# Kernel tuning notes

Hardware: AMD Instinct MI355X
Metric: run time of the kernel (lower is better)

Reference implementation:

```python
import jax, jax.numpy as jnp
import numpy as np

D_MODEL = 512
NHEAD = 8
HEAD_DIM = D_MODEL // NHEAD
A, B = 1024, 16


def setup_inputs() -> dict:
    key = jax.random.key(0)
    ks = jax.random.split(key, 6)
    s = 1.0 / np.sqrt(D_MODEL)
    return {
        "src": jax.random.normal(ks[0], (A, B, D_MODEL), jnp.float32),
        "asset_relation_bias": jax.random.normal(ks[1], (A, A), jnp.float32) * 0.1,
        "Wq": jax.random.normal(ks[2], (D_MODEL, D_MODEL), jnp.float32) * s,
        "bq": jnp.zeros((D_MODEL,), jnp.float32),
        "Wk": jax.random.normal(ks[3], (D_MODEL, D_MODEL), jnp.float32) * s,
        "bk": jnp.zeros((D_MODEL,), jnp.float32),
        "Wv": jax.random.normal(ks[4], (D_MODEL, D_MODEL), jnp.float32) * s,
        "bv": jnp.zeros((D_MODEL,), jnp.float32),
        "Wo": jax.random.normal(ks[5], (D_MODEL, D_MODEL), jnp.float32) * s,
        "bo": jnp.zeros((D_MODEL,), jnp.float32),
    }


def reference(src, asset_relation_bias, Wq, bq, Wk, bk, Wv, bv, Wo, bo):
    # src: [A, B, H]; attention is over the asset dim A.
    scale = HEAD_DIM ** -0.5

    def proj_heads(x, W, b):
        y = x @ W.T + b                      # [A, B, H]  (torch Linear: x @ W.T + b)
        y = y.reshape(A, B, NHEAD, HEAD_DIM)
        return jnp.transpose(y, (1, 2, 0, 3))  # [B, nh, A, hd]

    q = proj_heads(src, Wq, bq)
    k = proj_heads(src, Wk, bk)
    v = proj_heads(src, Wv, bv)

    logits = jnp.einsum("bnad,bnkd->bnak", q, k) * scale  # [B, nh, A, A]
    logits = logits + asset_relation_bias[None, None]     # additive relation bias
    attn = jax.nn.softmax(logits, axis=-1)                # dropout = identity (eval)
    out = jnp.einsum("bnak,bnkd->bnad", attn, v)          # [B, nh, A, hd]
    out = jnp.transpose(out, (2, 0, 1, 3)).reshape(A, B, D_MODEL)
    out = out @ Wo.T + bo
    return out
```

## Files before the change

kernel.cpp:

```cpp
#include <hip/hip_runtime.h>
#include <hip/hip_bf16.h>

#define A_DIM 1024
#define B_DIM 16
#define DM    512
#define NH    8
#define HD    64

#define LDT 72

typedef short s16x8 __attribute__((ext_vector_type(8)));
typedef float f32x4 __attribute__((ext_vector_type(4)));

static __device__ __forceinline__ unsigned short f2b(float f) {
    __hip_bfloat16 h = __float2bfloat16(f);
    unsigned short u;
    __builtin_memcpy(&u, &h, 2);
    return u;
}
static __device__ __forceinline__ uint2 cvt4(float4 v) {
    __hip_bfloat162 lo = __float22bfloat162_rn(make_float2(v.x, v.y));
    __hip_bfloat162 hi = __float22bfloat162_rn(make_float2(v.z, v.w));
    unsigned int ulo, uhi;
    __builtin_memcpy(&ulo, &lo, 4);
    __builtin_memcpy(&uhi, &hi, 4);
    return make_uint2(ulo, uhi);
}

__global__ __launch_bounds__(256) void qkv_gemm(
    const float* __restrict__ src,
    const float* __restrict__ Wq, const float* __restrict__ bq,
    const float* __restrict__ Wk, const float* __restrict__ bk,
    const float* __restrict__ Wv, const float* __restrict__ bv,
    short* __restrict__ Qb, short* __restrict__ Kb, short* __restrict__ Vb)
{
    __shared__ short As[128 * LDT];
    __shared__ short Bs[128 * LDT];

    const int tid  = threadIdx.x;
    const int wave = tid >> 6, lane = tid & 63;
    const int quad = lane >> 4, l16 = lane & 15;
    const int waveM = (wave >> 1) * 64, waveN = (wave & 1) * 64;
    const int mbase = blockIdx.y * 128;
    const int nbase = blockIdx.x * 128;
    const int mat   = nbase >> 9;
    const float* W    = (mat == 0) ? Wq : (mat == 1) ? Wk : Wv;
    const float* bvec = (mat == 0) ? bq : (mat == 1) ? bk : bv;
    short* dst        = (mat == 0) ? Qb : (mat == 1) ? Kb : Vb;
    const float oscale = (mat == 0) ? 0.125f : 1.0f;
    const int wrow0 = nbase & 511;

    f32x4 acc[4][4];
    #pragma unroll
    for (int i = 0; i < 4; i++)
        #pragma unroll
        for (int j = 0; j < 4; j++)
            acc[i][j] = (f32x4){0.f, 0.f, 0.f, 0.f};

    for (int kb = 0; kb < 8; ++kb) {
        __syncthreads();
        #pragma unroll
        for (int p = 0; p < 8; p++) {
            int chunk = tid + p * 256;
            int row = chunk >> 4, c = chunk & 15;
            float4 a4 = *(const float4*)&src[(mbase + row) * 512 + kb * 64 + c * 4];
            *(uint2*)&As[row * LDT + c * 4] = cvt4(a4);
            float4 w4 = *(const float4*)&W[(wrow0 + row) * 512 + kb * 64 + c * 4];
            *(uint2*)&Bs[row * LDT + c * 4] = cvt4(w4);
        }
        __syncthreads();
        #pragma unroll
        for (int k0i = 0; k0i < 2; k0i++) {
            s16x8 af[4], bf[4];
            #pragma unroll
            for (int mi = 0; mi < 4; mi++)
                af[mi] = *(const s16x8*)&As[(waveM + mi * 16 + l16) * LDT + (k0i * 4 + quad) * 8];
            #pragma unroll
            for (int ni = 0; ni < 4; ni++)
                bf[ni] = *(const s16x8*)&Bs[(waveN + ni * 16 + l16) * LDT + (k0i * 4 + quad) * 8];
            #pragma unroll
            for (int mi = 0; mi < 4; mi++)
                #pragma unroll
                for (int ni = 0; ni < 4; ni++)
                    acc[mi][ni] = __builtin_amdgcn_mfma_f32_16x16x32_bf16(
                        af[mi], bf[ni], acc[mi][ni], 0, 0, 0);
        }
    }

    #pragma unroll
    for (int mi = 0; mi < 4; mi++) {
        #pragma unroll
        for (int ni = 0; ni < 4; ni++) {
            #pragma unroll
            for (int r = 0; r < 4; r++) {
                int t = mbase + waveM + mi * 16 + quad * 4 + r;
                int o = wrow0 + waveN + ni * 16 + l16;
                float v = (acc[mi][ni][r] + bvec[o]) * oscale;
                int a = t >> 4, bb = t & 15, n = o >> 6, d = o & 63;
                dst[((bb * NH + n) * A_DIM + a) * HD + d] = (short)f2b(v);
            }
        }
    }
}

__global__ __launch_bounds__(256) void attn_kernel(
    const short* __restrict__ Qb, const short* __restrict__ Kb,
    const short* __restrict__ Vb, const float* __restrict__ bias,
    short* __restrict__ AO)
{
    __shared__ short Ks[64 * LDT];
    __shared__ short Vt[64 * LDT];
    __shared__ short Ps[4][16 * LDT];

    const int tid  = threadIdx.x;
    const int wave = tid >> 6, lane = tid & 63;
    const int quad = lane >> 4, l16 = lane & 15;
    const int bn = blockIdx.y;
    const int qrow0 = blockIdx.x * 64 + wave * 16;

    const short* Qg = Qb + bn * (A_DIM * HD);
    const short* Kg = Kb + bn * (A_DIM * HD);
    const short* Vg = Vb + bn * (A_DIM * HD);

    s16x8 qf[2];
    #pragma unroll
    for (int k0i = 0; k0i < 2; k0i++)
        qf[k0i] = *(const s16x8*)&Qg[(qrow0 + l16) * HD + k0i * 32 + quad * 8];

    float lsum[4];
    f32x4 of[4];
    #pragma unroll
    for (int r = 0; r < 4; r++) lsum[r] = 0.f;
    #pragma unroll
    for (int db = 0; db < 4; db++) of[db] = (f32x4){0.f, 0.f, 0.f, 0.f};

    for (int kb = 0; kb < 16; ++kb) {
        __syncthreads();
        #pragma unroll
        for (int p = 0; p < 2; p++) {
            int chunk = tid + p * 256;
            int row = chunk >> 3, c = chunk & 7;
            *(s16x8*)&Ks[row * LDT + c * 8] =
                *(const s16x8*)&Kg[(kb * 64 + row) * HD + c * 8];
            s16x8 vv = *(const s16x8*)&Vg[(kb * 64 + row) * HD + c * 8];
            #pragma unroll
            for (int j = 0; j < 8; j++) {
                int d = c * 8 + j;
                Vt[d * LDT + (((row >> 3) ^ c) << 3) + (row & 7)] = vv[j];
            }
        }
        __syncthreads();

        float sv[4][4];
        #pragma unroll
        for (int cb = 0; cb < 4; cb++) {
            f32x4 s = (f32x4){0.f, 0.f, 0.f, 0.f};
            #pragma unroll
            for (int k0i = 0; k0i < 2; k0i++) {
                s16x8 kf = *(const s16x8*)&Ks[(cb * 16 + l16) * LDT + (k0i * 4 + quad) * 8];
                s = __builtin_amdgcn_mfma_f32_16x16x32_bf16(qf[k0i], kf, s, 0, 0, 0);
            }
            #pragma unroll
            for (int r = 0; r < 4; r++) {
                int arow = qrow0 + quad * 4 + r;
                int kcol = kb * 64 + cb * 16 + l16;
                sv[cb][r] = s[r] + bias[arow * A_DIM + kcol];
            }
        }

        #pragma unroll
        for (int r = 0; r < 4; r++) {
            int prow = quad * 4 + r;
            #pragma unroll
            for (int cb = 0; cb < 4; cb++) {
                float pv = __expf(sv[cb][r]);
                lsum[r] += pv;
                Ps[wave][prow * LDT + cb * 16 + l16] = (short)f2b(pv);
            }
        }

        #pragma unroll
        for (int k0i = 0; k0i < 2; k0i++) {
            s16x8 pf = *(const s16x8*)&Ps[wave][l16 * LDT + (k0i * 4 + quad) * 8];
            #pragma unroll
            for (int db = 0; db < 4; db++) {
                int rr = db * 16 + l16;
                s16x8 vf = *(const s16x8*)&Vt[rr * LDT +
                            (((k0i * 4 + quad) ^ (rr >> 3)) << 3)];
                of[db] = __builtin_amdgcn_mfma_f32_16x16x32_bf16(pf, vf, of[db], 0, 0, 0);
            }
        }
    }

    #pragma unroll
    for (int r = 0; r < 4; r++) {
        float ps = lsum[r];
        ps += __shfl_xor(ps, 1);
        ps += __shfl_xor(ps, 2);
        ps += __shfl_xor(ps, 4);
        ps += __shfl_xor(ps, 8);
        lsum[r] = 1.0f / ps;
    }

    const int b = bn >> 3, n = bn & 7;
    #pragma unroll
    for (int db = 0; db < 4; db++) {
        #pragma unroll
        for (int r = 0; r < 4; r++) {
            int a = qrow0 + quad * 4 + r;
            int d = db * 16 + l16;
            float v = of[db][r] * lsum[r];
            AO[(a * B_DIM + b) * DM + n * HD + d] = (short)f2b(v);
        }
    }
}

__global__ __launch_bounds__(256) void out_gemm(
    const short* __restrict__ Xin,
    const float* __restrict__ Wo, const float* __restrict__ bo,
    float* __restrict__ out)
{
    __shared__ short As[128 * LDT];
    __shared__ short Bs[128 * LDT];

    const int tid  = threadIdx.x;
    const int wave = tid >> 6, lane = tid & 63;
    const int quad = lane >> 4, l16 = lane & 15;
    const int waveM = (wave >> 1) * 64, waveN = (wave & 1) * 64;
    const int mbase = blockIdx.y * 128;
    const int nbase = blockIdx.x * 128;

    f32x4 acc[4][4];
    #pragma unroll
    for (int i = 0; i < 4; i++)
        #pragma unroll
        for (int j = 0; j < 4; j++)
            acc[i][j] = (f32x4){0.f, 0.f, 0.f, 0.f};

    for (int kb = 0; kb < 8; ++kb) {
        __syncthreads();
        #pragma unroll
        for (int p = 0; p < 4; p++) {
            int chunk = tid + p * 256;
            int row = chunk >> 3, c = chunk & 7;
            *(s16x8*)&As[row * LDT + c * 8] =
                *(const s16x8*)&Xin[(mbase + row) * 512 + kb * 64 + c * 8];
        }
        #pragma unroll
        for (int p = 0; p < 8; p++) {
            int chunk = tid + p * 256;
            int row = chunk >> 4, c = chunk & 15;
            float4 w4 = *(const float4*)&Wo[(nbase + row) * 512 + kb * 64 + c * 4];
            *(uint2*)&Bs[row * LDT + c * 4] = cvt4(w4);
        }
        __syncthreads();
        #pragma unroll
        for (int k0i = 0; k0i < 2; k0i++) {
            s16x8 af[4], bf[4];
            #pragma unroll
            for (int mi = 0; mi < 4; mi++)
                af[mi] = *(const s16x8*)&As[(waveM + mi * 16 + l16) * LDT + (k0i * 4 + quad) * 8];
            #pragma unroll
            for (int ni = 0; ni < 4; ni++)
                bf[ni] = *(const s16x8*)&Bs[(waveN + ni * 16 + l16) * LDT + (k0i * 4 + quad) * 8];
            #pragma unroll
            for (int mi = 0; mi < 4; mi++)
                #pragma unroll
                for (int ni = 0; ni < 4; ni++)
                    acc[mi][ni] = __builtin_amdgcn_mfma_f32_16x16x32_bf16(
                        af[mi], bf[ni], acc[mi][ni], 0, 0, 0);
        }
    }

    #pragma unroll
    for (int mi = 0; mi < 4; mi++) {
        #pragma unroll
        for (int ni = 0; ni < 4; ni++) {
            #pragma unroll
            for (int r = 0; r < 4; r++) {
                int t = mbase + waveM + mi * 16 + quad * 4 + r;
                int o = nbase + waveN + ni * 16 + l16;
                out[t * 512 + o] = acc[mi][ni][r] + bo[o];
            }
        }
    }
}

extern "C" void kernel_launch(void* const* d_in, const int* in_sizes, int n_in,
                              void* d_out, int out_size, void* d_ws, size_t ws_size,
                              hipStream_t stream) {
    const float* src  = (const float*)d_in[0];
    const float* bias = (const float*)d_in[1];
    const float* Wq   = (const float*)d_in[2];
    const float* bq   = (const float*)d_in[3];
    const float* Wk   = (const float*)d_in[4];
    const float* bk   = (const float*)d_in[5];
    const float* Wv   = (const float*)d_in[6];
    const float* bv   = (const float*)d_in[7];
    const float* Wo   = (const float*)d_in[8];
    const float* bo   = (const float*)d_in[9];

    short* ws = (short*)d_ws;
    short* Qb = ws;
    short* Kb = ws + (size_t)(1 << 23);
    short* Vb = ws + (size_t)(2 << 23);

    const bool big_ws = ws_size >= (size_t)(64u << 20);
    short* AO = big_ws ? (ws + (size_t)3 * (1 << 23))
                       : (short*)d_out;

    qkv_gemm<<<dim3(12, 128), 256, 0, stream>>>(src, Wq, bq, Wk, bk, Wv, bv, Qb, Kb, Vb);
    attn_kernel<<<dim3(16, 128), 256, 0, stream>>>(Qb, Kb, Vb, bias, AO);

    if (big_ws) {
        out_gemm<<<dim3(4, 128), 256, 0, stream>>>(AO, Wo, bo, (float*)d_out);
    } else {
        float* Cs = (float*)d_ws;
        out_gemm<<<dim3(4, 128), 256, 0, stream>>>(AO, Wo, bo, Cs);
        (void)hipMemcpyAsync(d_out, Cs, (size_t)out_size * sizeof(float),
                             hipMemcpyDeviceToDevice, stream);
    }
}
```

Before: 251.4 us.

## Double-buffer K/V tiles, compute transposed scores to keep P in registers, use exp2

The attention kernel now double-buffers the K and V tiles in shared memory and prefetches the next tile into registers while the current one is processed, which removes one barrier per iteration. Scores are computed as K·Q^T, so each lane holds a row of probabilities that packs straight into the MFMA A operand, and the per-wave shared-memory P staging round trip is gone. Softmax uses exp2, with log2(e) folded into the Q scale and into a bias pre-scaled by a new small kernel; the bias is now read as float4 per lane. This adds an extra launch and a bias copy in the workspace, and V fragments are loaded as two 4-element halves.

```diff
diff --git a/kernel.cpp b/kernel.cpp
--- a/kernel.cpp
+++ b/kernel.cpp
@@ -6,10 +6,13 @@
 #define DM    512
 #define NH    8
 #define HD    64
+#define NTOK  (A_DIM * B_DIM)
 
 #define LDT 72
+#define LOG2E 1.44269504088896f
 
 typedef short s16x8 __attribute__((ext_vector_type(8)));
+typedef short s16x4 __attribute__((ext_vector_type(4)));
 typedef float f32x4 __attribute__((ext_vector_type(4)));
 
 static __device__ __forceinline__ unsigned short f2b(float f) {
@@ -18,13 +21,23 @@
     __builtin_memcpy(&u, &h, 2);
     return u;
 }
+static __device__ __forceinline__ unsigned int pk2(float a, float b) {
+    __hip_bfloat162 h = __float22bfloat162_rn(make_float2(a, b));
+    unsigned int u;
+    __builtin_memcpy(&u, &h, 4);
+    return u;
+}
 static __device__ __forceinline__ uint2 cvt4(float4 v) {
-    __hip_bfloat162 lo = __float22bfloat162_rn(make_float2(v.x, v.y));
-    __hip_bfloat162 hi = __float22bfloat162_rn(make_float2(v.z, v.w));
-    unsigned int ulo, uhi;
-    __builtin_memcpy(&ulo, &lo, 4);
-    __builtin_memcpy(&uhi, &hi, 4);
-    return make_uint2(ulo, uhi);
+    return make_uint2(pk2(v.x, v.y), pk2(v.z, v.w));
+}
+
+__global__ __launch_bounds__(256) void bias_scale(
+    const float* __restrict__ in, float* __restrict__ out)
+{
+    int i = (blockIdx.x * 256 + threadIdx.x) * 4;
+    float4 v = *(const float4*)&in[i];
+    v.x *= LOG2E; v.y *= LOG2E; v.z *= LOG2E; v.w *= LOG2E;
+    *(float4*)&out[i] = v;
 }
 
 __global__ __launch_bounds__(256) void qkv_gemm(
@@ -47,7 +60,7 @@
     const float* W    = (mat == 0) ? Wq : (mat == 1) ? Wk : Wv;
     const float* bvec = (mat == 0) ? bq : (mat == 1) ? bk : bv;
     short* dst        = (mat == 0) ? Qb : (mat == 1) ? Kb : Vb;
-    const float oscale = (mat == 0) ? 0.125f : 1.0f;
+    const float oscale = (mat == 0) ? 0.125f * LOG2E : 1.0f;
     const int wrow0 = nbase & 511;
 
     f32x4 acc[4][4];
@@ -105,102 +118,124 @@
 
 __global__ __launch_bounds__(256) void attn_kernel(
     const short* __restrict__ Qb, const short* __restrict__ Kb,
-    const short* __restrict__ Vb, const float* __restrict__ bias,
+    const short* __restrict__ Vb, const float* __restrict__ biasS,
     short* __restrict__ AO)
 {
-    __shared__ short Ks[64 * LDT];
-    __shared__ short Vt[64 * LDT];
-    __shared__ short Ps[4][16 * LDT];
+    __shared__ short Ks[2][64 * LDT];
+    __shared__ short Vt[2][64 * LDT];
 
     const int tid  = threadIdx.x;
-    const int wave = tid >> 6, lane = tid & 63;
+    const int lane = tid & 63;
+    const int wave = tid >> 6;
     const int quad = lane >> 4, l16 = lane & 15;
+    const int qh = quad >> 1, ql = quad & 1;
     const int bn = blockIdx.y;
     const int qrow0 = blockIdx.x * 64 + wave * 16;
 
     const short* Qg = Qb + bn * (A_DIM * HD);
     const short* Kg = Kb + bn * (A_DIM * HD);
     const short* Vg = Vb + bn * (A_DIM * HD);
+    const float* brow = biasS + (size_t)(qrow0 + l16) * A_DIM;
 
     s16x8 qf[2];
     #pragma unroll
     for (int k0i = 0; k0i < 2; k0i++)
         qf[k0i] = *(const s16x8*)&Qg[(qrow0 + l16) * HD + k0i * 32 + quad * 8];
 
-    float lsum[4];
+    const int row0 = tid >> 3, c0 = tid & 7;
+    const int row1 = (tid + 256) >> 3, c1 = c0;
+
+    float lsum = 0.f;
     f32x4 of[4];
     #pragma unroll
-    for (int r = 0; r < 4; r++) lsum[r] = 0.f;
-    #pragma unroll
     for (int db = 0; db < 4; db++) of[db] = (f32x4){0.f, 0.f, 0.f, 0.f};
 
+    {
+        s16x8 k0 = *(const s16x8*)&Kg[row0 * HD + c0 * 8];
+        s16x8 k1 = *(const s16x8*)&Kg[row1 * HD + c1 * 8];
+        s16x8 v0 = *(const s16x8*)&Vg[row0 * HD + c0 * 8];
+        s16x8 v1 = *(const s16x8*)&Vg[row1 * HD + c1 * 8];
+        *(s16x8*)&Ks[0][row0 * LDT + c0 * 8] = k0;
+        *(s16x8*)&Ks[0][row1 * LDT + c1 * 8] = k1;
+        #pragma unroll
+        for (int j = 0; j < 8; j++) {
+            Vt[0][(c0 * 8 + j) * LDT + (((row0 >> 3) ^ c0) << 3) + (row0 & 7)] = v0[j];
+            Vt[0][(c1 * 8 + j) * LDT + (((row1 >> 3) ^ c1) << 3) + (row1 & 7)] = v1[j];
+        }
+    }
+    __syncthreads();
+
     for (int kb = 0; kb < 16; ++kb) {
-        __syncthreads();
-        #pragma unroll
-        for (int p = 0; p < 2; p++) {
-            int chunk = tid + p * 256;
-            int row = chunk >> 3, c = chunk & 7;
-            *(s16x8*)&Ks[row * LDT + c * 8] =
-                *(const s16x8*)&Kg[(kb * 64 + row) * HD + c * 8];
-            s16x8 vv = *(const s16x8*)&Vg[(kb * 64 + row) * HD + c * 8];
-            #pragma unroll
-            for (int j = 0; j < 8; j++) {
-                int d = c * 8 + j;
-                Vt[d * LDT + (((row >> 3) ^ c) << 3) + (row & 7)] = vv[j];
-            }
-        }
-        __syncthreads();
-
-        float sv[4][4];
+        const int buf = kb & 1;
+
+        s16x8 kp0, kp1, vp0, vp1;
+        if (kb < 15) {
+            const short* Kn = Kg + (kb + 1) * 64 * HD;
+            const short* Vn = Vg + (kb + 1) * 64 * HD;
+            kp0 = *(const s16x8*)&Kn[row0 * HD + c0 * 8];
+            kp1 = *(const s16x8*)&Kn[row1 * HD + c1 * 8];
+            vp0 = *(const s16x8*)&Vn[row0 * HD + c0 * 8];
+            vp1 = *(const s16x8*)&Vn[row1 * HD + c1 * 8];
+        }
+
+        float pv[4][4];
         #pragma unroll
         for (int cb = 0; cb < 4; cb++) {
             f32x4 s = (f32x4){0.f, 0.f, 0.f, 0.f};
             #pragma unroll
             for (int k0i = 0; k0i < 2; k0i++) {
-                s16x8 kf = *(const s16x8*)&Ks[(cb * 16 + l16) * LDT + (k0i * 4 + quad) * 8];
-                s = __builtin_amdgcn_mfma_f32_16x16x32_bf16(qf[k0i], kf, s, 0, 0, 0);
+                s16x8 kf = *(const s16x8*)&Ks[buf][(cb * 16 + l16) * LDT + (k0i * 4 + quad) * 8];
+                s = __builtin_amdgcn_mfma_f32_16x16x32_bf16(kf, qf[k0i], s, 0, 0, 0);
             }
-            #pragma unroll
-            for (int r = 0; r < 4; r++) {
-                int arow = qrow0 + quad * 4 + r;
-                int kcol = kb * 64 + cb * 16 + l16;
-                sv[cb][r] = s[r] + bias[arow * A_DIM + kcol];
+            float4 bz = *(const float4*)&brow[kb * 64 + cb * 16 + quad * 4];
+            pv[cb][0] = __builtin_exp2f(s[0] + bz.x);
+            pv[cb][1] = __builtin_exp2f(s[1] + bz.y);
+            pv[cb][2] = __builtin_exp2f(s[2] + bz.z);
+            pv[cb][3] = __builtin_exp2f(s[3] + bz.w);
+            lsum += pv[cb][0] + pv[cb][1] + pv[cb][2] + pv[cb][3];
+        }
+
+        uint4 ua = make_uint4(pk2(pv[0][0], pv[0][1]), pk2(pv[0][2], pv[0][3]),
+                              pk2(pv[1][0], pv[1][1]), pk2(pv[1][2], pv[1][3]));
+        uint4 ub = make_uint4(pk2(pv[2][0], pv[2][1]), pk2(pv[2][2], pv[2][3]),
+                              pk2(pv[3][0], pv[3][1]), pk2(pv[3][2], pv[3][3]));
+        s16x8 pfA, pfB;
+        __builtin_memcpy(&pfA, &ua, 16);
+        __builtin_memcpy(&pfB, &ub, 16);
+
+        #pragma unroll
+        for (int db = 0; db < 4; db++) {
+            int dd = db * 16 + l16, d3 = dd >> 3;
+            int base = dd * LDT + ql * 4;
+            s16x4 v0 = *(const s16x4*)&Vt[buf][base + (((0 + qh) ^ d3) << 3)];
+            s16x4 v1 = *(const s16x4*)&Vt[buf][base + (((2 + qh) ^ d3) << 3)];
+            s16x8 vf01 = __builtin_shufflevector(v0, v1, 0, 1, 2, 3, 4, 5, 6, 7);
+            of[db] = __builtin_amdgcn_mfma_f32_16x16x32_bf16(pfA, vf01, of[db], 0, 0, 0);
+            s16x4 v2 = *(const s16x4*)&Vt[buf][base + (((4 + qh) ^ d3) << 3)];
+            s16x4 v3 = *(const s16x4*)&Vt[buf][base + (((6 + qh) ^ d3) << 3)];
+            s16x8 vf23 = __builtin_shufflevector(v2, v3, 0, 1, 2, 3, 4, 5, 6, 7);
+            of[db] = __builtin_amdgcn_mfma_f32_16x16x32_bf16(pfB, vf23, of[db], 0, 0, 0);
+        }
+
+        if (kb < 15) {
+            const int nb = buf ^ 1;
+            *(s16x8*)&Ks[nb][row0 * LDT + c0 * 8] = kp0;
+            *(s16x8*)&Ks[nb][row1 * LDT + c1 * 8] = kp1;
+            #pragma unroll
+            for (int j = 0; j < 8; j++) {
+                Vt[nb][(c0 * 8 + j) * LDT + (((row0 >> 3) ^ c0) << 3) + (row0 & 7)] = vp0[j];
+                Vt[nb][(c1 * 8 + j) * LDT + (((row1 >> 3) ^ c1) << 3) + (row1 & 7)] = vp1[j];
             }
         }
-
-        #pragma unroll
-        for (int r = 0; r < 4; r++) {
-            int prow = quad * 4 + r;
-            #pragma unroll
-            for (int cb = 0; cb < 4; cb++) {
-                float pv = __expf(sv[cb][r]);
-                lsum[r] += pv;
-                Ps[wave][prow * LDT + cb * 16 + l16] = (short)f2b(pv);
-            }
-        }
-
-        #pragma unroll
-        for (int k0i = 0; k0i < 2; k0i++) {
-            s16x8 pf = *(const s16x8*)&Ps[wave][l16 * LDT + (k0i * 4 + quad) * 8];
-            #pragma unroll
-            for (int db = 0; db < 4; db++) {
-                int rr = db * 16 + l16;
-                s16x8 vf = *(const s16x8*)&Vt[rr * LDT +
-                            (((k0i * 4 + quad) ^ (rr >> 3)) << 3)];
-                of[db] = __builtin_amdgcn_mfma_f32_16x16x32_bf16(pf, vf, of[db], 0, 0, 0);
-            }
-        }
-    }
-
-    #pragma unroll
-    for (int r = 0; r < 4; r++) {
-        float ps = lsum[r];
-        ps += __shfl_xor(ps, 1);
-        ps += __shfl_xor(ps, 2);
-        ps += __shfl_xor(ps, 4);
-        ps += __shfl_xor(ps, 8);
-        lsum[r] = 1.0f / ps;
-    }
+        __syncthreads();
+    }
+
+    lsum += __shfl_xor(lsum, 16);
+    lsum += __shfl_xor(lsum, 32);
+    float linv[4];
+    #pragma unroll
+    for (int r = 0; r < 4; r++)
+        linv[r] = 1.0f / __shfl(lsum, (lane & 48) | (quad * 4 + r));
 
     const int b = bn >> 3, n = bn & 7;
     #pragma unroll
@@ -209,8 +244,7 @@
         for (int r = 0; r < 4; r++) {
             int a = qrow0 + quad * 4 + r;
             int d = db * 16 + l16;
-            float v = of[db][r] * lsum[r];
-            AO[(a * B_DIM + b) * DM + n * HD + d] = (short)f2b(v);
+            AO[(a * B_DIM + b) * DM + n * HD + d] = (short)f2b(of[db][r] * linv[r]);
         }
     }
 }
@@ -305,12 +339,20 @@
     short* Kb = ws + (size_t)(1 << 23);
     short* Vb = ws + (size_t)(2 << 23);
 
-    const bool big_ws = ws_size >= (size_t)(64u << 20);
-    short* AO = big_ws ? (ws + (size_t)3 * (1 << 23))
-                       : (short*)d_out;
-
+    const bool big_ws = ws_size >= (size_t)(72u << 20);
+    float* biasS;
+    short* AO;
+    if (big_ws) {
+        biasS = (float*)(ws + (size_t)3 * (1 << 23));
+        AO    = ws + (size_t)3 * (1 << 23) + (size_t)(1 << 21);
+    } else {
+        AO    = (short*)d_out;
+        biasS = (float*)((short*)d_out + (size_t)NTOK * DM);
+    }
+
+    bias_scale<<<dim3(A_DIM * A_DIM / 1024), 256, 0, stream>>>(bias, biasS);
     qkv_gemm<<<dim3(12, 128), 256, 0, stream>>>(src, Wq, bq, Wk, bk, Wv, bv, Qb, Kb, Vb);
-    attn_kernel<<<dim3(16, 128), 256, 0, stream>>>(Qb, Kb, Vb, bias, AO);
+    attn_kernel<<<dim3(16, 128), 256, 0, stream>>>(Qb, Kb, Vb, biasS, AO);
 
     if (big_ws) {
         out_gemm<<<dim3(4, 128), 256, 0, stream>>>(AO, Wo, bo, (float*)d_out);
```

Result: slower. 262.6 us (+4.5%).
